# Optimization experiments

Hardware: AMD Instinct MI355X
Metric: run time of the kernel (lower is better)

Reference implementation:

```python
import jax, jax.numpy as jnp
import numpy as np

B, H, L, DK, S = 8, 8, 4096, 64, 512
GAMMA = 0.99

sg = jax.lax.stop_gradient

def st(x):  # straight-through: value 0, gradient passes
    return x - sg(x)


def setup_inputs() -> dict:
    key = jax.random.key(0)
    k1, k2 = jax.random.split(key, 2)
    vecs = jax.random.normal(k1, (B, H, L, DK), jnp.float32)
    c_sum = jax.random.normal(k2, (H, S, DK), jnp.float32)
    c_count = jnp.ones((H, S), jnp.float32)
    loss_mask = jnp.ones((B, L), jnp.float32)
    return dict(vecs=vecs, c_sum=c_sum, c_count=c_count, loss_mask=loss_mask,
                n_device=1, n_block_per_update=1)


def reference(vecs, c_sum, c_count, loss_mask, n_device, n_block_per_update):
    # codebook (stop-gradient, as in _get_codebook)
    c = sg(c_sum / jnp.clip(c_count[..., None], 0.01))  # [H,S,d]

    # get_shortcodes: squared distances via ||v||^2 - 2 v.c + ||c||^2
    v2 = jnp.sum(jnp.square(vecs), axis=-1)[..., None]          # [B,H,L,1]
    c2 = jnp.sum(jnp.square(c), axis=-1)[None, :, None, :]      # [1,H,1,S]
    diffs2 = v2 - 2.0 * jnp.einsum('bhlk,hsk->bhls', vecs, c) + c2
    z = jnp.argmin(diffs2, axis=-1).astype(jnp.int32)           # [B,H,L]
    errs2 = jax.nn.relu(jnp.min(diffs2, axis=-1))               # [B,H,L]

    # get_codewords: gather chosen codewords per head
    cz = jnp.take_along_axis(c[None], z[..., None], axis=2)     # [B,H,L,d]

    # straight-through quantized output
    vecs_hat = sg(cz) + st(vecs)

    # commitment loss
    l_commit = jnp.mean(jnp.sum(loss_mask[:, None, :] * errs2, axis=1))

    # EMA codebook targets (scatter-accumulate instead of one-hot einsum; same math)
    dp = n_device * n_block_per_update
    mask = loss_mask[:, None, :]                                # [B,1,L]
    mvecs = vecs * mask[..., None]                              # [B,H,L,d]
    head_ids = jnp.arange(H, dtype=jnp.int32)[None, :, None]
    flat_ids = (z + S * head_ids).reshape(-1)                   # [B*H*L]
    c_sum_hat = dp * jax.ops.segment_sum(
        mvecs.reshape(-1, DK), flat_ids, num_segments=H * S).reshape(H, S, DK)
    c_count_hat = dp * jax.ops.segment_sum(
        jnp.broadcast_to(mask, (B, H, L)).reshape(-1), flat_ids,
        num_segments=H * S).reshape(H, S)
    c_sum_tgt = (1.0 - GAMMA) * c_sum_hat + GAMMA * c_sum
    c_count_tgt = (1.0 - GAMMA) * c_count_hat + GAMMA * c_count

    l_codebook = (jnp.sum(sg(c_sum - c_sum_tgt) * st(c_sum))
                  + jnp.sum(sg(c_count - c_count_tgt) * st(c_count)))

    return vecs_hat, z, l_commit, l_codebook, errs2
```

## Files before the change

kernel.cpp:

```cpp
#include <hip/hip_runtime.h>
#include <hip/hip_bf16.h>


#define Bc 8
#define Hc 8
#define Lc 4096
#define DKc 64
#define Sc 512

typedef __attribute__((ext_vector_type(8))) short bf16x8;
typedef __attribute__((ext_vector_type(8))) unsigned short u16x8;
typedef __attribute__((ext_vector_type(4))) float f32x4;

#define WS_C_OFF    0u
#define WS_C2_OFF   1048576u
#define WS_CBH_OFF  1064960u
#define WS_CBL_OFF  1589248u
#define WS_PART_OFF 2113536u
#define NPART       8192

__device__ __forceinline__ unsigned short f32_to_bf16_rne(float x) {
    unsigned u = __float_as_uint(x);
    unsigned r = (u + 0x7FFFu + ((u >> 16) & 1u)) >> 16;
    return (unsigned short)r;
}
__device__ __forceinline__ float bf16_hi_f32(unsigned short h) {
    return __uint_as_float(((unsigned)h) << 16);
}

__global__ __launch_bounds__(256) void prep_kernel(
        const float* __restrict__ c_sum,
        const float* __restrict__ c_count,
        float* __restrict__ c,
        float* __restrict__ c2,
        unsigned short* __restrict__ cbh,
        unsigned short* __restrict__ cbl) {
    int row  = (blockIdx.x * blockDim.x + threadIdx.x) >> 6;
    int lane = threadIdx.x & 63;
    float cnt = c_count[row];
    float inv = 1.0f / fmaxf(cnt, 0.01f);
    float val = c_sum[row * DKc + lane] * inv;
    c[row * DKc + lane] = val;
    float v16 = val * 16.0f;
    unsigned short hi = f32_to_bf16_rne(v16);
    unsigned short lo = f32_to_bf16_rne(v16 - bf16_hi_f32(hi));
    int s = row & (Sc - 1);
    size_t hbase = (size_t)(row >> 9) * (Sc * 128);
    int boff = (s * 128 + lane * 2) ^ ((s & 7) << 4);
    *(unsigned short*)((char*)cbh + hbase + boff) = hi;
    *(unsigned short*)((char*)cbl + hbase + boff) = lo;
    float sq = val * val;
    #pragma unroll
    for (int off = 32; off; off >>= 1) sq += __shfl_xor(sq, off);
    if (lane == 0) c2[row] = sq;
}

__global__ __launch_bounds__(256, 4) void vq_mfma_kernel(
        const float* __restrict__ vecs,
        const float* __restrict__ c,
        const float* __restrict__ c2,
        const unsigned short* __restrict__ cbh,
        const unsigned short* __restrict__ cbl,
        const float* __restrict__ loss_mask,
        float* __restrict__ out_vh,
        float* __restrict__ out_z,
        float* __restrict__ out_err,
        float* __restrict__ partials) {
    __shared__ unsigned short bhi[2][32 * DKc];
    __shared__ unsigned short blo[2][32 * DKc];
    __shared__ float c2_lds[Sc];
    __shared__ int2  top2s[128];

    const int t   = threadIdx.x;
    const int l   = t & 63;
    const int w   = t >> 6;
    const int col = l & 15;
    const int ksl = l >> 4;

    const int flat = blockIdx.x;
    const int h    = flat & 7;
    const int idx  = flat >> 3;
    const int b    = idx >> 5;
    const int lt   = idx & 31;
    const int bh   = b * Hc + h;

    const float* Avec  = vecs + ((size_t)bh * Lc + (size_t)lt * 128) * DKc;
    const float* Bp    = c + (size_t)h * Sc * DKc;
    const char*  cbh_h = (const char*)cbh + (size_t)h * (Sc * 128);
    const char*  cbl_h = (const char*)cbl + (size_t)h * (Sc * 128);

    u16x8 nh, nl;
    {
        nh = *(const u16x8*)(cbh_h + w * 1024 + l * 16);
        nl = *(const u16x8*)(cbl_h + w * 1024 + l * 16);
    }

    bf16x8 fah[2][2], fal[2][2];
    #pragma unroll
    for (int rt = 0; rt < 2; ++rt) {
        const float* Ar = Avec + (size_t)((w << 5) + (rt << 4) + col) * DKc;
        #pragma unroll
        for (int ks = 0; ks < 2; ++ks) {
            int k0 = (ks << 5) + (ksl << 3);
            float4 p0 = *reinterpret_cast<const float4*>(Ar + k0);
            float4 p1 = *reinterpret_cast<const float4*>(Ar + k0 + 4);
            float e8[8] = {p0.x, p0.y, p0.z, p0.w, p1.x, p1.y, p1.z, p1.w};
            bf16x8 hv, lv;
            #pragma unroll
            for (int i = 0; i < 8; ++i) {
                float v16 = e8[i] * 16.0f;
                unsigned short hi = f32_to_bf16_rne(v16);
                hv[i] = (short)hi;
                lv[i] = (short)f32_to_bf16_rne(v16 - bf16_hi_f32(hi));
            }
            fah[rt][ks] = hv;
            fal[rt][ks] = lv;
        }
    }

    c2_lds[t]       = c2[h * Sc + t];
    c2_lds[t + 256] = c2[h * Sc + t + 256];

    *(u16x8*)((char*)bhi[0] + w * 1024 + l * 16) = nh;
    *(u16x8*)((char*)blo[0] + w * 1024 + l * 16) = nl;
    __syncthreads();

    unsigned v1k[2][4], v2k[2][4];
    #pragma unroll
    for (int rt = 0; rt < 2; ++rt)
        #pragma unroll
        for (int r = 0; r < 4; ++r) { v1k[rt][r] = 0u; v2k[rt][r] = 0u; }

    for (int chunk = 0; chunk < 16; ++chunk) {
        if (chunk < 15) {
            nh = *(const u16x8*)(cbh_h + ((chunk + 1) << 12) + w * 1024 + l * 16);
            nl = *(const u16x8*)(cbl_h + ((chunk + 1) << 12) + w * 1024 + l * 16);
        }
        const char* ph = (const char*)bhi[chunk & 1];
        const char* pl = (const char*)blo[chunk & 1];

        auto INIT = [&](int j, f32x4 (&cA)[2], f32x4 (&cB)[2]) {
            float m0 = fmaf(-128.0f, c2_lds[(chunk << 5) + (j << 4) + col], 65536.0f);
            cA[0] = (f32x4){m0, m0, m0, m0};
            cA[1] = (f32x4){m0, m0, m0, m0};
            cB[0] = (f32x4){0.f, 0.f, 0.f, 0.f};
            cB[1] = (f32x4){0.f, 0.f, 0.f, 0.f};
        };
        auto STEP = [&](int j, f32x4 (&cA)[2], f32x4 (&cB)[2]) {
            int crow = (j << 4) + col;
            int o0 = ((crow << 7) + (ksl << 4)) ^ ((col & 7) << 4);
            bf16x8 h0 = *reinterpret_cast<const bf16x8*>(ph + o0);
            bf16x8 h1 = *reinterpret_cast<const bf16x8*>(ph + (o0 ^ 64));
            bf16x8 g0 = *reinterpret_cast<const bf16x8*>(pl + o0);
            bf16x8 g1 = *reinterpret_cast<const bf16x8*>(pl + (o0 ^ 64));
            #pragma unroll
            for (int rt = 0; rt < 2; ++rt) {
                cA[rt] = __builtin_amdgcn_mfma_f32_16x16x32_bf16(fah[rt][0], h0, cA[rt], 0, 0, 0);
                cB[rt] = __builtin_amdgcn_mfma_f32_16x16x32_bf16(fal[rt][0], h0, cB[rt], 0, 0, 0);
                cA[rt] = __builtin_amdgcn_mfma_f32_16x16x32_bf16(fah[rt][1], h1, cA[rt], 0, 0, 0);
                cB[rt] = __builtin_amdgcn_mfma_f32_16x16x32_bf16(fal[rt][1], h1, cB[rt], 0, 0, 0);
                cA[rt] = __builtin_amdgcn_mfma_f32_16x16x32_bf16(fah[rt][0], g0, cA[rt], 0, 0, 0);
                cB[rt] = __builtin_amdgcn_mfma_f32_16x16x32_bf16(fah[rt][1], g1, cB[rt], 0, 0, 0);
            }
        };
        auto FOLD = [&](int j, f32x4 (&cA)[2], f32x4 (&cB)[2]) {
            unsigned invc = 511u - (unsigned)((chunk << 5) + (j << 4) + col);
            #pragma unroll
            for (int rt = 0; rt < 2; ++rt)
                #pragma unroll
                for (int r = 0; r < 4; ++r) {
                    float m = cA[rt][r] + cB[rt][r];
                    unsigned ki  = (unsigned)(int)m;
                    unsigned key = (ki << 9) + invc;
                    unsigned a = key > v2k[rt][r] ? key : v2k[rt][r];
                    v2k[rt][r] = a < v1k[rt][r] ? a : v1k[rt][r];
                    v1k[rt][r] = key > v1k[rt][r] ? key : v1k[rt][r];
                }
        };

        f32x4 sA0[2], sB0[2], sA1[2], sB1[2];
        INIT(0, sA0, sB0); STEP(0, sA0, sB0);
        INIT(1, sA1, sB1); STEP(1, sA1, sB1);
        FOLD(0, sA0, sB0);
        FOLD(1, sA1, sB1);

        if (chunk < 15) {
            *(u16x8*)((char*)bhi[(chunk + 1) & 1] + w * 1024 + l * 16) = nh;
            *(u16x8*)((char*)blo[(chunk + 1) & 1] + w * 1024 + l * 16) = nl;
            __syncthreads();
        }
    }

    #pragma unroll
    for (int off = 1; off <= 8; off <<= 1) {
        #pragma unroll
        for (int rt = 0; rt < 2; ++rt)
            #pragma unroll
            for (int r = 0; r < 4; ++r) {
                unsigned o1 = (unsigned)__shfl_xor((int)v1k[rt][r], off);
                unsigned o2 = (unsigned)__shfl_xor((int)v2k[rt][r], off);
                unsigned lo = min(v1k[rt][r], o1);
                v1k[rt][r]  = max(v1k[rt][r], o1);
                v2k[rt][r]  = max(lo, max(v2k[rt][r], o2));
            }
    }
    if (col == 0) {
        #pragma unroll
        for (int rt = 0; rt < 2; ++rt)
            #pragma unroll
            for (int r = 0; r < 4; ++r) {
                unsigned k1 = v1k[rt][r], k2 = v2k[rt][r];
                int z1 = 511 - (int)(k1 & 0x1FFu);
                int z2 = 511 - (int)(k2 & 0x1FFu);
                bool need = ((k1 >> 9) - (k2 >> 9)) < 13u;
                top2s[(w << 5) + (rt << 4) + (ksl << 2) + r] = make_int2(z1, need ? z2 : z1);
            }
    }
    __syncthreads();

    const int qo = (l & 15) << 2;
    const int rq = l >> 4;
    double macc = 0.0;
    #pragma unroll
    for (int it = 0; it < 8; ++it) {
        int  rloc = (w << 5) + (it << 2) + rq;
        int  lrow = lt * 128 + rloc;
        long grow = (long)bh * Lc + lrow;
        int2 zz   = top2s[rloc];
        const float* Ar = Avec + (size_t)rloc * DKc;
        const float* C1 = Bp + (size_t)zz.x * DKc;
        const float* C2 = Bp + (size_t)zz.y * DKc;
        f32x4 va = *reinterpret_cast<const f32x4*>(Ar + qo);
        f32x4 ca = *reinterpret_cast<const f32x4*>(C1 + qo);
        f32x4 cb = *reinterpret_cast<const f32x4*>(C2 + qo);
        double dd = 0.0;
        if (zz.x != zz.y) {
            #pragma unroll
            for (int m = 0; m < 4; ++m) {
                double a = (double)ca[m], bb = (double)cb[m], vv = (double)va[m];
                dd = fma(a - bb, (a + bb) - 2.0 * vv, dd);
            }
            dd += __shfl_xor(dd, 1);
            dd += __shfl_xor(dd, 2);
            dd += __shfl_xor(dd, 4);
            dd += __shfl_xor(dd, 8);
        }
        bool second = (dd > 0.0) || (dd == 0.0 && zz.y < zz.x);
        int zsel = second ? zz.y : zz.x;
        f32x4 cs = second ? cb : ca;
        float e = 0.f;
        #pragma unroll
        for (int m = 0; m < 4; ++m) {
            float td = va[m] - cs[m];
            e = fmaf(td, td, e);
        }
        e += __shfl_xor(e, 1);
        e += __shfl_xor(e, 2);
        e += __shfl_xor(e, 4);
        e += __shfl_xor(e, 8);
        *reinterpret_cast<f32x4*>(out_vh + (size_t)grow * DKc + qo) = cs;
        if ((l & 15) == 0) {
            out_z[grow]   = (float)zsel;
            out_err[grow] = e;
            macc += (double)loss_mask[b * Lc + lrow] * (double)e;
        }
    }
    macc += __shfl_xor(macc, 16);
    macc += __shfl_xor(macc, 32);
    if (l == 0) partials[flat * 4 + w] = (float)macc;
}

__global__ __launch_bounds__(256) void finalize_kernel(
        const float* __restrict__ partials, int n,
        float* __restrict__ out_lcommit, float* __restrict__ out_lcode) {
    __shared__ double sh[256];
    double a = 0.0;
    for (int i = threadIdx.x; i < n; i += 256) a += (double)partials[i];
    sh[threadIdx.x] = a;
    __syncthreads();
    for (int s = 128; s; s >>= 1) {
        if (threadIdx.x < s) sh[threadIdx.x] += sh[threadIdx.x + s];
        __syncthreads();
    }
    if (threadIdx.x == 0) {
        double lc = sh[0] / (double)(Bc * Lc);
        *out_lcommit = (float)lc;
        *out_lcode   = 0.0f;
    }
}

extern "C" void kernel_launch(void* const* d_in, const int* in_sizes, int n_in,
                              void* d_out, int out_size, void* d_ws, size_t ws_size,
                              hipStream_t stream) {
    const float* vecs      = (const float*)d_in[0];
    const float* c_sum     = (const float*)d_in[1];
    const float* c_count   = (const float*)d_in[2];
    const float* loss_mask = (const float*)d_in[3];
    (void)in_sizes; (void)n_in; (void)out_size; (void)ws_size;

    char* ws = (char*)d_ws;
    float*          c        = (float*)(ws + WS_C_OFF);
    float*          c2       = (float*)(ws + WS_C2_OFF);
    unsigned short* cbh      = (unsigned short*)(ws + WS_CBH_OFF);
    unsigned short* cbl      = (unsigned short*)(ws + WS_CBL_OFF);
    float*          partials = (float*)(ws + WS_PART_OFF);

    float* out = (float*)d_out;
    float* out_vh      = out;
    float* out_z       = out + (size_t)Bc * Hc * Lc * DKc;
    float* out_lcommit = out_z + (size_t)Bc * Hc * Lc;
    float* out_lcode   = out_lcommit + 1;
    float* out_err     = out_lcode + 1;

    prep_kernel<<<(Hc * Sc * 64) / 256, 256, 0, stream>>>(c_sum, c_count, c, c2, cbh, cbl);

    vq_mfma_kernel<<<2048, 256, 0, stream>>>(vecs, c, c2, cbh, cbl, loss_mask,
                                             out_vh, out_z, out_err, partials);

    finalize_kernel<<<1, 256, 0, stream>>>(partials, NPART, out_lcommit, out_lcode);
}
```

Before: 89.34 us.

## Prefetch codebook two chunks ahead and merge split MFMA accumulators

Global loads of the bf16 hi/lo codebook chunks are issued two iterations ahead using two register sets, instead of one, so more global latency is hidden behind the MFMA work. The two separate accumulator chains (cA/cB) are merged into a single chain per row tile, which drops the final add and frees accumulator registers. The cost is a longer serial dependency chain of six MFMAs per accumulator, which can expose MFMA latency, plus extra registers for the second prefetch buffer.

Result: slower. 93.25 us (+4.4%).

```diff
diff --git a/kernel.cpp b/kernel.cpp
--- a/kernel.cpp
+++ b/kernel.cpp
@@ -89,11 +89,9 @@
     const char*  cbh_h = (const char*)cbh + (size_t)h * (Sc * 128);
     const char*  cbl_h = (const char*)cbl + (size_t)h * (Sc * 128);
 
-    u16x8 nh, nl;
-    {
-        nh = *(const u16x8*)(cbh_h + w * 1024 + l * 16);
-        nl = *(const u16x8*)(cbl_h + w * 1024 + l * 16);
-    }
+    u16x8 nh0, nl0, nh1, nl1;
+    nh0 = *(const u16x8*)(cbh_h + w * 1024 + l * 16);
+    nl0 = *(const u16x8*)(cbl_h + w * 1024 + l * 16);
 
     bf16x8 fah[2][2], fal[2][2];
     #pragma unroll
@@ -121,8 +119,10 @@
     c2_lds[t]       = c2[h * Sc + t];
     c2_lds[t + 256] = c2[h * Sc + t + 256];
 
-    *(u16x8*)((char*)bhi[0] + w * 1024 + l * 16) = nh;
-    *(u16x8*)((char*)blo[0] + w * 1024 + l * 16) = nl;
+    *(u16x8*)((char*)bhi[0] + w * 1024 + l * 16) = nh0;
+    *(u16x8*)((char*)blo[0] + w * 1024 + l * 16) = nl0;
+    nh1 = *(const u16x8*)(cbh_h + (1 << 12) + w * 1024 + l * 16);
+    nl1 = *(const u16x8*)(cbl_h + (1 << 12) + w * 1024 + l * 16);
     __syncthreads();
 
     unsigned v1k[2][4], v2k[2][4];
@@ -132,21 +132,24 @@
         for (int r = 0; r < 4; ++r) { v1k[rt][r] = 0u; v2k[rt][r] = 0u; }
 
     for (int chunk = 0; chunk < 16; ++chunk) {
-        if (chunk < 15) {
-            nh = *(const u16x8*)(cbh_h + ((chunk + 1) << 12) + w * 1024 + l * 16);
-            nl = *(const u16x8*)(cbl_h + ((chunk + 1) << 12) + w * 1024 + l * 16);
+        if (chunk < 14) {
+            if ((chunk & 1) == 0) {
+                nh0 = *(const u16x8*)(cbh_h + ((chunk + 2) << 12) + w * 1024 + l * 16);
+                nl0 = *(const u16x8*)(cbl_h + ((chunk + 2) << 12) + w * 1024 + l * 16);
+            } else {
+                nh1 = *(const u16x8*)(cbh_h + ((chunk + 2) << 12) + w * 1024 + l * 16);
+                nl1 = *(const u16x8*)(cbl_h + ((chunk + 2) << 12) + w * 1024 + l * 16);
+            }
         }
         const char* ph = (const char*)bhi[chunk & 1];
         const char* pl = (const char*)blo[chunk & 1];
 
-        auto INIT = [&](int j, f32x4 (&cA)[2], f32x4 (&cB)[2]) {
+        auto INIT = [&](int j, f32x4 (&cA)[2]) {
             float m0 = fmaf(-128.0f, c2_lds[(chunk << 5) + (j << 4) + col], 65536.0f);
             cA[0] = (f32x4){m0, m0, m0, m0};
             cA[1] = (f32x4){m0, m0, m0, m0};
-            cB[0] = (f32x4){0.f, 0.f, 0.f, 0.f};
-            cB[1] = (f32x4){0.f, 0.f, 0.f, 0.f};
         };
-        auto STEP = [&](int j, f32x4 (&cA)[2], f32x4 (&cB)[2]) {
+        auto STEP = [&](int j, f32x4 (&cA)[2]) {
             int crow = (j << 4) + col;
             int o0 = ((crow << 7) + (ksl << 4)) ^ ((col & 7) << 4);
             bf16x8 h0 = *reinterpret_cast<const bf16x8*>(ph + o0);
@@ -156,20 +159,20 @@
             #pragma unroll
             for (int rt = 0; rt < 2; ++rt) {
                 cA[rt] = __builtin_amdgcn_mfma_f32_16x16x32_bf16(fah[rt][0], h0, cA[rt], 0, 0, 0);
-                cB[rt] = __builtin_amdgcn_mfma_f32_16x16x32_bf16(fal[rt][0], h0, cB[rt], 0, 0, 0);
                 cA[rt] = __builtin_amdgcn_mfma_f32_16x16x32_bf16(fah[rt][1], h1, cA[rt], 0, 0, 0);
-                cB[rt] = __builtin_amdgcn_mfma_f32_16x16x32_bf16(fal[rt][1], h1, cB[rt], 0, 0, 0);
+                cA[rt] = __builtin_amdgcn_mfma_f32_16x16x32_bf16(fal[rt][0], h0, cA[rt], 0, 0, 0);
+                cA[rt] = __builtin_amdgcn_mfma_f32_16x16x32_bf16(fal[rt][1], h1, cA[rt], 0, 0, 0);
                 cA[rt] = __builtin_amdgcn_mfma_f32_16x16x32_bf16(fah[rt][0], g0, cA[rt], 0, 0, 0);
-                cB[rt] = __builtin_amdgcn_mfma_f32_16x16x32_bf16(fah[rt][1], g1, cB[rt], 0, 0, 0);
+                cA[rt] = __builtin_amdgcn_mfma_f32_16x16x32_bf16(fah[rt][1], g1, cA[rt], 0, 0, 0);
             }
         };
-        auto FOLD = [&](int j, f32x4 (&cA)[2], f32x4 (&cB)[2]) {
+        auto FOLD = [&](int j, f32x4 (&cA)[2]) {
             unsigned invc = 511u - (unsigned)((chunk << 5) + (j << 4) + col);
             #pragma unroll
             for (int rt = 0; rt < 2; ++rt)
                 #pragma unroll
                 for (int r = 0; r < 4; ++r) {
-                    float m = cA[rt][r] + cB[rt][r];
+                    float m = cA[rt][r];
                     unsigned ki  = (unsigned)(int)m;
                     unsigned key = (ki << 9) + invc;
                     unsigned a = key > v2k[rt][r] ? key : v2k[rt][r];
@@ -178,15 +181,20 @@
                 }
         };
 
-        f32x4 sA0[2], sB0[2], sA1[2], sB1[2];
-        INIT(0, sA0, sB0); STEP(0, sA0, sB0);
-        INIT(1, sA1, sB1); STEP(1, sA1, sB1);
-        FOLD(0, sA0, sB0);
-        FOLD(1, sA1, sB1);
+        f32x4 sA0[2], sA1[2];
+        INIT(0, sA0); STEP(0, sA0);
+        INIT(1, sA1); STEP(1, sA1);
+        FOLD(0, sA0);
+        FOLD(1, sA1);
 
         if (chunk < 15) {
-            *(u16x8*)((char*)bhi[(chunk + 1) & 1] + w * 1024 + l * 16) = nh;
-            *(u16x8*)((char*)blo[(chunk + 1) & 1] + w * 1024 + l * 16) = nl;
+            if (((chunk + 1) & 1) == 0) {
+                *(u16x8*)((char*)bhi[0] + w * 1024 + l * 16) = nh0;
+                *(u16x8*)((char*)blo[0] + w * 1024 + l * 16) = nl0;
+            } else {
+                *(u16x8*)((char*)bhi[1] + w * 1024 + l * 16) = nh1;
+                *(u16x8*)((char*)blo[1] + w * 1024 + l * 16) = nl1;
+            }
             __syncthreads();
         }
     }
```
